# Kernel optimization log

Measured on AMD Instinct MI355X. Metric: run time of the kernel, lower is better.

## Reference

```python
import jax, jax.numpy as jnp
import numpy as np

V, H, E, L = 50257, 1024, 1024, 2048


def setup_inputs() -> dict:
    key = jax.random.key(0)
    ks = jax.random.split(key, 13)
    s = 0.05
    return {
        'y_i': jax.random.randint(ks[0], (1, 1), 0, V),
        'h_i': jax.random.normal(ks[1], (1, 1, H), jnp.float32),
        'cnn_a': jax.random.normal(ks[2], (1, H, L), jnp.float32),
        'cnn_c': jax.random.normal(ks[3], (1, H, L), jnp.float32),
        'emb': jax.random.normal(ks[4], (V, H), jnp.float32) * s,
        'W_t': jax.random.normal(ks[5], (E, H), jnp.float32) * s,
        'b_t': jax.random.normal(ks[6], (E,), jnp.float32) * s,
        'W_ih': jax.random.normal(ks[7], (3 * H, H + E), jnp.float32) * s,
        'W_hh': jax.random.normal(ks[8], (3 * H, H), jnp.float32) * s,
        'b_ih': jax.random.normal(ks[9], (3 * H,), jnp.float32) * s,
        'b_hh': jax.random.normal(ks[10], (3 * H,), jnp.float32) * s,
        'W_o': jax.random.normal(ks[11], (V, H), jnp.float32) * s,
        'b_o': jax.random.normal(ks[12], (V,), jnp.float32) * s,
    }


def reference(y_i, h_i, cnn_a, cnn_c, emb, W_t, b_t, W_ih, W_hh, b_ih, b_hh, W_o, b_o):
    # g_i = embedding(y_i); dropout is identity in eval mode
    g = emb[y_i]                                   # [1,1,H]
    # d_i = Linear(h_i) + g_i
    d = h_i @ W_t.T + b_t + g                      # [1,1,E]
    # attention: softmax(bmm(d_i, cnn_a))
    scores = jnp.einsum('bte,bel->btl', d, cnn_a).reshape(1, -1)  # [1,L]
    a = jax.nn.softmax(scores, axis=-1)
    # c_i = bmm(a, cnn_c^T)
    c = jnp.einsum('btl,bhl->bth', a.reshape(1, 1, -1), cnn_c)    # [1,1,H]
    # single-step, single-layer GRU (PyTorch gate order: r, z, n)
    x = jnp.concatenate((g, c), axis=-1)[0]        # [1, H+E]
    h0 = h_i[0]                                    # [1, H]
    gx = x @ W_ih.T + b_ih                         # [1, 3H]
    gh = h0 @ W_hh.T + b_hh                        # [1, 3H]
    r = jax.nn.sigmoid(gx[:, :H] + gh[:, :H])
    z = jax.nn.sigmoid(gx[:, H:2 * H] + gh[:, H:2 * H])
    n = jnp.tanh(gx[:, 2 * H:] + r * gh[:, 2 * H:])
    h_new = (1.0 - z) * n + z * h0                 # [1, H]
    gru_hidden = h_new[None]                       # [1,1,H]
    # output distribution
    logits = h_new @ W_o.T + b_o                   # [1, V]
    softmax_output = jax.nn.log_softmax(logits, axis=-1)
    return (softmax_output, gru_hidden)
```

## Files before the change

kernel.cpp:

```cpp
#include <hip/hip_runtime.h>
#include <math.h>

#define Hn 1024
#define En 1024
#define Ln 2048
#define Vn 50257

__device__ __forceinline__ float waveReduceSum(float v) {
#pragma unroll
    for (int off = 32; off > 0; off >>= 1)
        v += __shfl_down(v, off, 64);
    return v;
}

__device__ __forceinline__ float waveReduceMax(float v) {
#pragma unroll
    for (int off = 32; off > 0; off >>= 1)
        v = fmaxf(v, __shfl_down(v, off, 64));
    return v;
}

__global__ __launch_bounds__(256) void k_d_scores(
    const float* __restrict__ h_i, const float* __restrict__ W_t,
    const float* __restrict__ b_t, const float* __restrict__ emb,
    const int* __restrict__ y, const float* __restrict__ cnn_a,
    float* __restrict__ part) {
    __shared__ float dsh[64];
    const int t = threadIdx.x, wave = t >> 6, lane = t & 63;
    const int e0 = blockIdx.y * 64;
    const float4* h4 = (const float4*)h_i;
    float4 hfrag[4];
#pragma unroll
    for (int k = 0; k < 4; ++k) hfrag[k] = h4[lane + k * 64];
    const int yy = y[0];
#pragma unroll 4
    for (int rr = 0; rr < 16; ++rr) {
        const int row = wave * 16 + rr;
        const float4* wrow = (const float4*)(W_t + (size_t)(e0 + row) * Hn);
        float acc = 0.f;
#pragma unroll
        for (int k = 0; k < 4; ++k) {
            const float4 w = wrow[lane + k * 64];
            acc += w.x * hfrag[k].x + w.y * hfrag[k].y +
                   w.z * hfrag[k].z + w.w * hfrag[k].w;
        }
        acc = waveReduceSum(acc);
        if (lane == 0)
            dsh[row] = acc + b_t[e0 + row] + emb[(size_t)yy * Hn + e0 + row];
    }
    __syncthreads();
    const int l = blockIdx.x * 256 + t;
    float acc = 0.f;
#pragma unroll 8
    for (int e = 0; e < 64; ++e)
        acc += dsh[e] * cnn_a[(size_t)(e0 + e) * Ln + l];
    part[(size_t)blockIdx.y * Ln + l] = acc;
}

__global__ __launch_bounds__(256) void k_softmax_c(
    const float* __restrict__ part, const float* __restrict__ cnn_c,
    float* __restrict__ c) {
    __shared__ float red[4];
    __shared__ float bc;
    const int t = threadIdx.x, wave = t >> 6, lane = t & 63;
    const int h = blockIdx.x;
    const float4* p4 = (const float4*)part;
    float4 r0 = {0.f, 0.f, 0.f, 0.f}, r1 = {0.f, 0.f, 0.f, 0.f};
#pragma unroll
    for (int p = 0; p < 16; ++p) {
        const float4 a = p4[p * 512 + t];
        const float4 b = p4[p * 512 + 256 + t];
        r0.x += a.x; r0.y += a.y; r0.z += a.z; r0.w += a.w;
        r1.x += b.x; r1.y += b.y; r1.z += b.z; r1.w += b.w;
    }
    float m = fmaxf(fmaxf(fmaxf(r0.x, r0.y), fmaxf(r0.z, r0.w)),
                    fmaxf(fmaxf(r1.x, r1.y), fmaxf(r1.z, r1.w)));
    m = waveReduceMax(m);
    if (lane == 0) red[wave] = m;
    __syncthreads();
    if (t == 0) bc = fmaxf(fmaxf(red[0], red[1]), fmaxf(red[2], red[3]));
    __syncthreads();
    const float M = bc;
    const float e0 = expf(r0.x - M), e1 = expf(r0.y - M);
    const float e2 = expf(r0.z - M), e3 = expf(r0.w - M);
    const float e4 = expf(r1.x - M), e5 = expf(r1.y - M);
    const float e6 = expf(r1.z - M), e7 = expf(r1.w - M);
    float s = e0 + e1 + e2 + e3 + e4 + e5 + e6 + e7;
    s = waveReduceSum(s);
    if (lane == 0) red[wave] = s;
    __syncthreads();
    if (t == 0) bc = red[0] + red[1] + red[2] + red[3];
    __syncthreads();
    const float inv = 1.0f / bc;
    const float4* crow = (const float4*)(cnn_c + (size_t)h * Ln);
    const float4 w0 = crow[t], w1 = crow[t + 256];
    float pc = e0 * w0.x + e1 * w0.y + e2 * w0.z + e3 * w0.w +
               e4 * w1.x + e5 * w1.y + e6 * w1.z + e7 * w1.w;
    pc = waveReduceSum(pc);
    if (lane == 0) red[wave] = pc;
    __syncthreads();
    if (t == 0) c[h] = (red[0] + red[1] + red[2] + red[3]) * inv;
}

__global__ __launch_bounds__(256) void k_gru_fused(
    const float* __restrict__ emb, const int* __restrict__ y,
    const float* __restrict__ c, const float* __restrict__ h0,
    const float* __restrict__ W_ih, const float* __restrict__ W_hh,
    const float* __restrict__ b_ih, const float* __restrict__ b_hh,
    float* __restrict__ out_h) {
    __shared__ float redx[3][4], redh[3][4];
    const int t = threadIdx.x, wave = t >> 6, lane = t & 63;
    const int i = blockIdx.x;
    const float* g = emb + (size_t)y[0] * Hn;
    const float4 gv = ((const float4*)g)[t];
    const float4 cv = ((const float4*)c)[t];
    const float4 hv = ((const float4*)h0)[t];
    float ax[3], ah[3];
#pragma unroll
    for (int j = 0; j < 3; ++j) {
        const float4* wih = (const float4*)(W_ih + (size_t)(j * Hn + i) * (Hn + En));
        const float4 w0 = wih[t];
        const float4 w1 = wih[t + 256];
        ax[j] = w0.x * gv.x + w0.y * gv.y + w0.z * gv.z + w0.w * gv.w +
                w1.x * cv.x + w1.y * cv.y + w1.z * cv.z + w1.w * cv.w;
        const float4* whh = (const float4*)(W_hh + (size_t)(j * Hn + i) * Hn);
        const float4 w2 = whh[t];
        ah[j] = w2.x * hv.x + w2.y * hv.y + w2.z * hv.z + w2.w * hv.w;
    }
#pragma unroll
    for (int j = 0; j < 3; ++j) {
        ax[j] = waveReduceSum(ax[j]);
        ah[j] = waveReduceSum(ah[j]);
    }
    if (lane == 0) {
#pragma unroll
        for (int j = 0; j < 3; ++j) { redx[j][wave] = ax[j]; redh[j][wave] = ah[j]; }
    }
    __syncthreads();
    if (t == 0) {
        float gx[3], gh[3];
#pragma unroll
        for (int j = 0; j < 3; ++j) {
            gx[j] = redx[j][0] + redx[j][1] + redx[j][2] + redx[j][3] + b_ih[j * Hn + i];
            gh[j] = redh[j][0] + redh[j][1] + redh[j][2] + redh[j][3] + b_hh[j * Hn + i];
        }
        const float r = 1.f / (1.f + expf(-(gx[0] + gh[0])));
        const float z = 1.f / (1.f + expf(-(gx[1] + gh[1])));
        const float n = tanhf(gx[2] + r * gh[2]);
        out_h[i] = (1.f - z) * n + z * h0[i];
    }
}

__global__ __launch_bounds__(1024) void k_logits(
    const float* __restrict__ W_o, const float* __restrict__ b_o,
    const float* __restrict__ hn, float* __restrict__ logits) {
    __shared__ float hsh[Hn];
    const int t = threadIdx.x;
    if (t < 256) ((float4*)hsh)[t] = ((const float4*)hn)[t];
    __syncthreads();
    const int wid = t >> 6, lane = t & 63;
    const int v = blockIdx.x * 16 + wid;
    if (v >= Vn) return;
    const float4* row = (const float4*)(W_o + (size_t)v * Hn);
    const float4* h4 = (const float4*)hsh;
    float acc = 0.f;
#pragma unroll
    for (int j = 0; j < 4; ++j) {
        const float4 w = row[lane + j * 64];
        const float4 hv = h4[lane + j * 64];
        acc += w.x * hv.x + w.y * hv.y + w.z * hv.z + w.w * hv.w;
    }
    acc = waveReduceSum(acc);
    if (lane == 0) logits[v] = acc + b_o[v];
}

__global__ __launch_bounds__(1024) void k_logsoftmax(float* __restrict__ out) {
    __shared__ float red[16];
    __shared__ float bc;
    const int t = threadIdx.x;
    float4* o4 = (float4*)out;
    const int N4 = Vn / 4;
    float m = -INFINITY;
    for (int i = t; i < N4; i += 1024) {
        const float4 v = o4[i];
        m = fmaxf(m, fmaxf(fmaxf(v.x, v.y), fmaxf(v.z, v.w)));
    }
    if (t == 0) m = fmaxf(m, out[Vn - 1]);
    m = waveReduceMax(m);
    if ((t & 63) == 0) red[t >> 6] = m;
    __syncthreads();
    if (t == 0) {
        float mm = red[0];
#pragma unroll
        for (int i = 1; i < 16; ++i) mm = fmaxf(mm, red[i]);
        bc = mm;
    }
    __syncthreads();
    const float M = bc;
    float s = 0.f;
    for (int i = t; i < N4; i += 1024) {
        const float4 v = o4[i];
        s += expf(v.x - M) + expf(v.y - M) + expf(v.z - M) + expf(v.w - M);
    }
    if (t == 0) s += expf(out[Vn - 1] - M);
    s = waveReduceSum(s);
    if ((t & 63) == 0) red[t >> 6] = s;
    __syncthreads();
    if (t == 0) {
        float ss = 0.f;
#pragma unroll
        for (int i = 0; i < 16; ++i) ss += red[i];
        bc = M + logf(ss);
    }
    __syncthreads();
    const float lse = bc;
    for (int i = t; i < N4; i += 1024) {
        float4 v = o4[i];
        v.x -= lse; v.y -= lse; v.z -= lse; v.w -= lse;
        o4[i] = v;
    }
    if (t == 0) out[Vn - 1] -= lse;
}

extern "C" void kernel_launch(void* const* d_in, const int* in_sizes, int n_in,
                              void* d_out, int out_size, void* d_ws, size_t ws_size,
                              hipStream_t stream) {
    const int*   y     = (const int*)d_in[0];
    const float* h_i   = (const float*)d_in[1];
    const float* cnn_a = (const float*)d_in[2];
    const float* cnn_c = (const float*)d_in[3];
    const float* emb   = (const float*)d_in[4];
    const float* W_t   = (const float*)d_in[5];
    const float* b_t   = (const float*)d_in[6];
    const float* W_ih  = (const float*)d_in[7];
    const float* W_hh  = (const float*)d_in[8];
    const float* b_ih  = (const float*)d_in[9];
    const float* b_hh  = (const float*)d_in[10];
    const float* W_o   = (const float*)d_in[11];
    const float* b_o   = (const float*)d_in[12];
    float* out = (float*)d_out;

    float* ws    = (float*)d_ws;
    float* part  = ws;
    float* c_vec = part + 16 * Ln;

    float* out_h = out + Vn;

    k_d_scores<<<dim3(8, 16), dim3(256), 0, stream>>>(h_i, W_t, b_t, emb, y,
                                                      cnn_a, part);
    k_softmax_c<<<dim3(Hn), dim3(256), 0, stream>>>(part, cnn_c, c_vec);
    k_gru_fused<<<dim3(Hn), dim3(256), 0, stream>>>(emb, y, c_vec, h_i, W_ih,
                                                    W_hh, b_ih, b_hh, out_h);
    k_logits<<<dim3((Vn + 15) / 16), dim3(1024), 0, stream>>>(W_o, b_o, out_h, out);
    k_logsoftmax<<<dim3(1), dim3(1024), 0, stream>>>(out);
}
```

Measured before the change: 458.6 us.

## Hoist c-independent GRU matvecs into front kernel and parallelize log-softmax

Moves the W_hh·h and the embedding half of W_ih·x matvecs into the first kernel, so they run alongside the attention-score computation. The GRU finish kernel then only does the context-dependent half. Logits blocks now emit per-block max/sum-exp partials, and a multi-block finalize kernel merges them online and subtracts the logsumexp in parallel. This replaces the single-block three-pass log-softmax over 50K elements. The cost is extra workspace traffic and every finalize block redundantly reducing ~3142 partials.

After: 447.1 us. 2.5% less time.

```diff
diff --git a/kernel.cpp b/kernel.cpp
--- a/kernel.cpp
+++ b/kernel.cpp
@@ -5,6 +5,7 @@
 #define En 1024
 #define Ln 2048
 #define Vn 50257
+#define NLOGBLK ((Vn + 15) / 16)
 
 __device__ __forceinline__ float waveReduceSum(float v) {
 #pragma unroll
@@ -20,41 +21,73 @@
     return v;
 }
 
-__global__ __launch_bounds__(256) void k_d_scores(
+__global__ __launch_bounds__(256) void k_front(
     const float* __restrict__ h_i, const float* __restrict__ W_t,
     const float* __restrict__ b_t, const float* __restrict__ emb,
     const int* __restrict__ y, const float* __restrict__ cnn_a,
-    float* __restrict__ part) {
+    const float* __restrict__ W_ih, const float* __restrict__ W_hh,
+    const float* __restrict__ b_ih, const float* __restrict__ b_hh,
+    float* __restrict__ part, float* __restrict__ gxg, float* __restrict__ ghv) {
     __shared__ float dsh[64];
+    const int b = blockIdx.x;
     const int t = threadIdx.x, wave = t >> 6, lane = t & 63;
-    const int e0 = blockIdx.y * 64;
-    const float4* h4 = (const float4*)h_i;
-    float4 hfrag[4];
-#pragma unroll
-    for (int k = 0; k < 4; ++k) hfrag[k] = h4[lane + k * 64];
-    const int yy = y[0];
+    if (b < 128) {
+        const int ec = b >> 3, lc = b & 7;
+        const int e0 = ec * 64;
+        const float4* h4 = (const float4*)h_i;
+        float4 hfrag[4];
+#pragma unroll
+        for (int k = 0; k < 4; ++k) hfrag[k] = h4[lane + k * 64];
+        const int yy = y[0];
 #pragma unroll 4
-    for (int rr = 0; rr < 16; ++rr) {
-        const int row = wave * 16 + rr;
-        const float4* wrow = (const float4*)(W_t + (size_t)(e0 + row) * Hn);
+        for (int rr = 0; rr < 16; ++rr) {
+            const int row = wave * 16 + rr;
+            const float4* wrow = (const float4*)(W_t + (size_t)(e0 + row) * Hn);
+            float acc = 0.f;
+#pragma unroll
+            for (int k = 0; k < 4; ++k) {
+                const float4 w = wrow[lane + k * 64];
+                acc += w.x * hfrag[k].x + w.y * hfrag[k].y +
+                       w.z * hfrag[k].z + w.w * hfrag[k].w;
+            }
+            acc = waveReduceSum(acc);
+            if (lane == 0)
+                dsh[row] = acc + b_t[e0 + row] + emb[(size_t)yy * Hn + e0 + row];
+        }
+        __syncthreads();
+        const int l = lc * 256 + t;
         float acc = 0.f;
-#pragma unroll
-        for (int k = 0; k < 4; ++k) {
-            const float4 w = wrow[lane + k * 64];
-            acc += w.x * hfrag[k].x + w.y * hfrag[k].y +
-                   w.z * hfrag[k].z + w.w * hfrag[k].w;
-        }
-        acc = waveReduceSum(acc);
-        if (lane == 0)
-            dsh[row] = acc + b_t[e0 + row] + emb[(size_t)yy * Hn + e0 + row];
-    }
-    __syncthreads();
-    const int l = blockIdx.x * 256 + t;
-    float acc = 0.f;
 #pragma unroll 8
-    for (int e = 0; e < 64; ++e)
-        acc += dsh[e] * cnn_a[(size_t)(e0 + e) * Ln + l];
-    part[(size_t)blockIdx.y * Ln + l] = acc;
+        for (int e = 0; e < 64; ++e)
+            acc += dsh[e] * cnn_a[(size_t)(e0 + e) * Ln + l];
+        part[(size_t)ec * Ln + l] = acc;
+    } else {
+        const bool isB = (b < 512);
+        const int rbase = (isB ? (b - 128) : (b - 512)) * 8;
+        const float* xv = isB ? (emb + (size_t)y[0] * Hn) : h_i;
+        const float4* x4 = (const float4*)xv;
+        float4 xf[4];
+#pragma unroll
+        for (int k = 0; k < 4; ++k) xf[k] = x4[lane + k * 64];
+        const size_t pitch = isB ? (size_t)(Hn + En) : (size_t)Hn;
+        const float* Wm = isB ? W_ih : W_hh;
+        const float* bias = isB ? b_ih : b_hh;
+        float* outv = isB ? gxg : ghv;
+#pragma unroll
+        for (int rr = 0; rr < 2; ++rr) {
+            const int r = rbase + wave * 2 + rr;
+            const float4* wrow = (const float4*)(Wm + (size_t)r * pitch);
+            float acc = 0.f;
+#pragma unroll
+            for (int k = 0; k < 4; ++k) {
+                const float4 w = wrow[lane + k * 64];
+                acc += w.x * xf[k].x + w.y * xf[k].y +
+                       w.z * xf[k].z + w.w * xf[k].w;
+            }
+            acc = waveReduceSum(acc);
+            if (lane == 0) outv[r] = acc + bias[r];
+        }
+    }
 }
 
 __global__ __launch_bounds__(256) void k_softmax_c(
@@ -102,47 +135,35 @@
     if (t == 0) c[h] = (red[0] + red[1] + red[2] + red[3]) * inv;
 }
 
-__global__ __launch_bounds__(256) void k_gru_fused(
-    const float* __restrict__ emb, const int* __restrict__ y,
+__global__ __launch_bounds__(256) void k_gru_fin(
     const float* __restrict__ c, const float* __restrict__ h0,
-    const float* __restrict__ W_ih, const float* __restrict__ W_hh,
-    const float* __restrict__ b_ih, const float* __restrict__ b_hh,
+    const float* __restrict__ W_ih,
+    const float* __restrict__ gxg, const float* __restrict__ ghv,
     float* __restrict__ out_h) {
-    __shared__ float redx[3][4], redh[3][4];
+    __shared__ float red[3][4];
     const int t = threadIdx.x, wave = t >> 6, lane = t & 63;
     const int i = blockIdx.x;
-    const float* g = emb + (size_t)y[0] * Hn;
-    const float4 gv = ((const float4*)g)[t];
     const float4 cv = ((const float4*)c)[t];
-    const float4 hv = ((const float4*)h0)[t];
-    float ax[3], ah[3];
+    float a3[3];
 #pragma unroll
     for (int j = 0; j < 3; ++j) {
-        const float4* wih = (const float4*)(W_ih + (size_t)(j * Hn + i) * (Hn + En));
-        const float4 w0 = wih[t];
-        const float4 w1 = wih[t + 256];
-        ax[j] = w0.x * gv.x + w0.y * gv.y + w0.z * gv.z + w0.w * gv.w +
-                w1.x * cv.x + w1.y * cv.y + w1.z * cv.z + w1.w * cv.w;
-        const float4* whh = (const float4*)(W_hh + (size_t)(j * Hn + i) * Hn);
-        const float4 w2 = whh[t];
-        ah[j] = w2.x * hv.x + w2.y * hv.y + w2.z * hv.z + w2.w * hv.w;
-    }
-#pragma unroll
-    for (int j = 0; j < 3; ++j) {
-        ax[j] = waveReduceSum(ax[j]);
-        ah[j] = waveReduceSum(ah[j]);
-    }
+        const float4* wrow =
+            (const float4*)(W_ih + (size_t)(j * Hn + i) * (Hn + En) + Hn);
+        const float4 w = wrow[t];
+        a3[j] = w.x * cv.x + w.y * cv.y + w.z * cv.z + w.w * cv.w;
+    }
+#pragma unroll
+    for (int j = 0; j < 3; ++j) a3[j] = waveReduceSum(a3[j]);
     if (lane == 0) {
-#pragma unroll
-        for (int j = 0; j < 3; ++j) { redx[j][wave] = ax[j]; redh[j][wave] = ah[j]; }
+        red[0][wave] = a3[0]; red[1][wave] = a3[1]; red[2][wave] = a3[2];
     }
     __syncthreads();
     if (t == 0) {
         float gx[3], gh[3];
 #pragma unroll
         for (int j = 0; j < 3; ++j) {
-            gx[j] = redx[j][0] + redx[j][1] + redx[j][2] + redx[j][3] + b_ih[j * Hn + i];
-            gh[j] = redh[j][0] + redh[j][1] + redh[j][2] + redh[j][3] + b_hh[j * Hn + i];
+            gx[j] = red[j][0] + red[j][1] + red[j][2] + red[j][3] + gxg[j * Hn + i];
+            gh[j] = ghv[j * Hn + i];
         }
         const float r = 1.f / (1.f + expf(-(gx[0] + gh[0])));
         const float z = 1.f / (1.f + expf(-(gx[1] + gh[1])));
@@ -153,73 +174,88 @@
 
 __global__ __launch_bounds__(1024) void k_logits(
     const float* __restrict__ W_o, const float* __restrict__ b_o,
-    const float* __restrict__ hn, float* __restrict__ logits) {
+    const float* __restrict__ hn, float* __restrict__ logits,
+    float2* __restrict__ blk_ms) {
     __shared__ float hsh[Hn];
+    __shared__ float lsh[16];
     const int t = threadIdx.x;
     if (t < 256) ((float4*)hsh)[t] = ((const float4*)hn)[t];
     __syncthreads();
     const int wid = t >> 6, lane = t & 63;
     const int v = blockIdx.x * 16 + wid;
-    if (v >= Vn) return;
-    const float4* row = (const float4*)(W_o + (size_t)v * Hn);
-    const float4* h4 = (const float4*)hsh;
-    float acc = 0.f;
-#pragma unroll
-    for (int j = 0; j < 4; ++j) {
-        const float4 w = row[lane + j * 64];
-        const float4 hv = h4[lane + j * 64];
-        acc += w.x * hv.x + w.y * hv.y + w.z * hv.z + w.w * hv.w;
-    }
-    acc = waveReduceSum(acc);
-    if (lane == 0) logits[v] = acc + b_o[v];
-}
-
-__global__ __launch_bounds__(1024) void k_logsoftmax(float* __restrict__ out) {
-    __shared__ float red[16];
+    float logit = -INFINITY;
+    if (v < Vn) {
+        const float4* row = (const float4*)(W_o + (size_t)v * Hn);
+        const float4* h4 = (const float4*)hsh;
+        float acc = 0.f;
+#pragma unroll
+        for (int j = 0; j < 4; ++j) {
+            const float4 w = row[lane + j * 64];
+            const float4 hv = h4[lane + j * 64];
+            acc += w.x * hv.x + w.y * hv.y + w.z * hv.z + w.w * hv.w;
+        }
+        acc = waveReduceSum(acc);
+        if (lane == 0) {
+            logit = acc + b_o[v];
+            logits[v] = logit;
+        }
+    }
+    if (lane == 0) lsh[wid] = logit;
+    __syncthreads();
+    if (t == 0) {
+        float m = lsh[0];
+#pragma unroll
+        for (int i = 1; i < 16; ++i) m = fmaxf(m, lsh[i]);
+        float s = 0.f;
+#pragma unroll
+        for (int i = 0; i < 16; ++i) s += expf(lsh[i] - m);
+        blk_ms[blockIdx.x] = make_float2(m, s);
+    }
+}
+
+__global__ __launch_bounds__(1024) void k_lsm_fin(
+    const float2* __restrict__ blk_ms, float* __restrict__ out) {
+    __shared__ float red_m[16], red_s[16];
     __shared__ float bc;
     const int t = threadIdx.x;
+    float m = -INFINITY, s = 0.f;
+    for (int i = t; i < NLOGBLK; i += 1024) {
+        const float2 p = blk_ms[i];
+        const float M = fmaxf(m, p.x);
+        s = s * expf(m - M) + p.y * expf(p.x - M);
+        m = M;
+    }
+#pragma unroll
+    for (int off = 32; off > 0; off >>= 1) {
+        const float om = __shfl_down(m, off, 64);
+        const float os = __shfl_down(s, off, 64);
+        const float M = fmaxf(m, om);
+        s = s * expf(m - M) + os * expf(om - M);
+        m = M;
+    }
+    if ((t & 63) == 0) { red_m[t >> 6] = m; red_s[t >> 6] = s; }
+    __syncthreads();
+    if (t == 0) {
+        float M = red_m[0], S = red_s[0];
+#pragma unroll
+        for (int i = 1; i < 16; ++i) {
+            const float M2 = fmaxf(M, red_m[i]);
+            S = S * expf(M - M2) + red_s[i] * expf(red_m[i] - M2);
+            M = M2;
+        }
+        bc = M + logf(S);
+    }
+    __syncthreads();
+    const float lse = bc;
+    const int N4 = Vn / 4;
+    const int i = blockIdx.x * 1024 + t;
     float4* o4 = (float4*)out;
-    const int N4 = Vn / 4;
-    float m = -INFINITY;
-    for (int i = t; i < N4; i += 1024) {
-        const float4 v = o4[i];
-        m = fmaxf(m, fmaxf(fmaxf(v.x, v.y), fmaxf(v.z, v.w)));
-    }
-    if (t == 0) m = fmaxf(m, out[Vn - 1]);
-    m = waveReduceMax(m);
-    if ((t & 63) == 0) red[t >> 6] = m;
-    __syncthreads();
-    if (t == 0) {
-        float mm = red[0];
-#pragma unroll
-        for (int i = 1; i < 16; ++i) mm = fmaxf(mm, red[i]);
-        bc = mm;
-    }
-    __syncthreads();
-    const float M = bc;
-    float s = 0.f;
-    for (int i = t; i < N4; i += 1024) {
-        const float4 v = o4[i];
-        s += expf(v.x - M) + expf(v.y - M) + expf(v.z - M) + expf(v.w - M);
-    }
-    if (t == 0) s += expf(out[Vn - 1] - M);
-    s = waveReduceSum(s);
-    if ((t & 63) == 0) red[t >> 6] = s;
-    __syncthreads();
-    if (t == 0) {
-        float ss = 0.f;
-#pragma unroll
-        for (int i = 0; i < 16; ++i) ss += red[i];
-        bc = M + logf(ss);
-    }
-    __syncthreads();
-    const float lse = bc;
-    for (int i = t; i < N4; i += 1024) {
+    if (i < N4) {
         float4 v = o4[i];
         v.x -= lse; v.y -= lse; v.z -= lse; v.w -= lse;
         o4[i] = v;
     }
-    if (t == 0) out[Vn - 1] -= lse;
+    if (blockIdx.x == 0 && t == 0) out[Vn - 1] -= lse;
 }
 
 extern "C" void kernel_launch(void* const* d_in, const int* in_sizes, int n_in,
@@ -240,17 +276,20 @@
     const float* b_o   = (const float*)d_in[12];
     float* out = (float*)d_out;
 
-    float* ws    = (float*)d_ws;
-    float* part  = ws;
-    float* c_vec = part + 16 * Ln;
+    float*  ws     = (float*)d_ws;
+    float*  part   = ws;
+    float*  c_vec  = part + 16 * Ln;
+    float*  gxg    = c_vec + Hn;
+    float*  ghv    = gxg + 3 * Hn;
+    float2* blk_ms = (float2*)(ghv + 3 * Hn);
 
     float* out_h = out + Vn;
 
-    k_d_scores<<<dim3(8, 16), dim3(256), 0, stream>>>(h_i, W_t, b_t, emb, y,
-                                                      cnn_a, part);
+    k_front<<<dim3(896), dim3(256), 0, stream>>>(h_i, W_t, b_t, emb, y, cnn_a,
+                                                 W_ih, W_hh, b_ih, b_hh,
+                                                 part, gxg, ghv);
     k_softmax_c<<<dim3(Hn), dim3(256), 0, stream>>>(part, cnn_c, c_vec);
-    k_gru_fused<<<dim3(Hn), dim3(256), 0, stream>>>(emb, y, c_vec, h_i, W_ih,
-                                                    W_hh, b_ih, b_hh, out_h);
-    k_logits<<<dim3((Vn + 15) / 16), dim3(1024), 0, stream>>>(W_o, b_o, out_h, out);
-    k_logsoftmax<<<dim3(1), dim3(1024), 0, stream>>>(out);
-}
+    k_gru_fin<<<dim3(Hn), dim3(256), 0, stream>>>(c_vec, h_i, W_ih, gxg, ghv, out_h);
+    k_logits<<<dim3(NLOGBLK), dim3(1024), 0, stream>>>(W_o, b_o, out_h, out, blk_ms);
+    k_lsm_fin<<<dim3((Vn / 4 + 1023) / 1024), dim3(1024), 0, stream>>>(blk_ms, out);
+}
```
